# Performance work log

Hardware: AMD Instinct MI355X
Metric: run time of the kernel (lower is better)

## Reference

```python
import jax, jax.numpy as jnp
import numpy as np

ARITY = 4
DEPTH = 8  # leaves live at level DEPTH; levels 0..DEPTH, BFS layout
N_NODES = (ARITY ** (DEPTH + 1) - 1) // (ARITY - 1)  # 87381
V, E, H = 1024, 128, 128


def _offset(level):
    return (ARITY ** level - 1) // (ARITY - 1)


def _lstm_final(seq, w_ih, w_hh, b):
    # seq: [T, B, E_in] -> final hidden state [B, H] (torch LSTM cell, gate order i,f,g,o)
    B = seq.shape[1]
    Hh = w_hh.shape[1]
    xg = jnp.einsum('tbe,ge->tbg', seq, w_ih) + b  # precompute input projections [T,B,4H]

    def step(carry, g_t):
        h, c = carry
        g = g_t + h @ w_hh.T
        i, f, gg, o = jnp.split(g, 4, axis=-1)
        c = jax.nn.sigmoid(f) * c + jax.nn.sigmoid(i) * jnp.tanh(gg)
        h = jax.nn.sigmoid(o) * jnp.tanh(c)
        return (h, c), None

    init = (jnp.zeros((B, Hh), seq.dtype), jnp.zeros((B, Hh), seq.dtype))
    (h, _), _ = jax.lax.scan(step, init, xg)
    return h


def setup_inputs():
    key = jax.random.key(0)
    ks = jax.random.split(key, 12)
    s = 0.1
    labels = jax.random.randint(ks[0], (N_NODES,), 0, V)
    emb = jax.random.normal(ks[1], (V, E), jnp.float32) * s
    emb = emb.at[0].set(0.0)  # padding_idx=0
    mk = lambda k, shp: jax.random.normal(k, shp, jnp.float32) * s
    return {
        'labels': labels, 'emb': emb,
        'w_ih_f': mk(ks[2], (4 * H, E)), 'w_hh_f': mk(ks[3], (4 * H, H)),
        'b_ih_f': mk(ks[4], (4 * H,)), 'b_hh_f': mk(ks[5], (4 * H,)),
        'w_ih_b': mk(ks[6], (4 * H, E)), 'w_hh_b': mk(ks[7], (4 * H, H)),
        'b_ih_b': mk(ks[8], (4 * H,)), 'b_hh_b': mk(ks[9], (4 * H,)),
        'lin_w': mk(ks[10], (E, 2 * H)), 'lin_b': mk(ks[11], (E,)),
    }


def reference(labels, emb, w_ih_f, w_hh_f, b_ih_f, b_hh_f,
              w_ih_b, w_hh_b, b_ih_b, b_hh_b, lin_w, lin_b):
    # padding row is frozen at zero (padding_idx=0 semantics)
    emb = emb.at[0].set(0.0)
    node_emb = emb[labels]  # [N, E]
    bf = b_ih_f + b_hh_f
    bb = b_ih_b + b_hh_b
    enc = jnp.zeros((N_NODES, E), node_emb.dtype)
    # level-by-level dynamic batching: identical math to per-node recursion
    for level in range(DEPTH, -1, -1):
        start = _offset(level)
        count = ARITY ** level
        x = node_emb[start:start + count]  # [C, E]
        if level == DEPTH:
            seq = jnp.stack([x, x])  # leaves: [node, node] -> [2, C, E]
        else:
            cstart = _offset(level + 1)
            ch = enc[cstart:cstart + count * ARITY]
            ch = ch.reshape(count, ARITY, E).transpose(1, 0, 2)  # [K, C, E]
            seq = jnp.concatenate([x[None], ch, x[None]], axis=0)  # [K+2, C, E]
        h_f = _lstm_final(seq, w_ih_f, w_hh_f, bf)          # forward direction
        h_b = _lstm_final(seq[::-1], w_ih_b, w_hh_b, bb)    # reverse direction
        out = jnp.tanh(jnp.concatenate([h_f, h_b], axis=-1) @ lin_w.T + lin_b)
        enc = enc.at[start:start + count].set(out)
    return enc[0]  # root encoding, shape [E]
```

## Files before the change

### kernel.cpp

```cpp
#include <hip/hip_runtime.h>
#include <hip/hip_bf16.h>

typedef __attribute__((ext_vector_type(8))) short bf16x8;
typedef __attribute__((ext_vector_type(4))) float f32x4;

__device__ __forceinline__ ushort f2bf(float f) {
  union { float f; unsigned u; } v; v.f = f;
  unsigned u = v.u;
  return (ushort)((u + 0x7FFFu + ((u >> 16) & 1u)) >> 16);
}
__device__ __forceinline__ float bf2f(ushort u) {
  union { unsigned u; float f; } v; v.u = ((unsigned)u) << 16;
  return v.f;
}
__device__ __forceinline__ float fsig(float x) {
  return __builtin_amdgcn_rcpf(1.0f + __expf(-x));
}
__device__ __forceinline__ float ftnh(float x) {
  float e = __expf(2.0f * x);
  return 1.0f - 2.0f * __builtin_amdgcn_rcpf(e + 1.0f);
}
__device__ __forceinline__ f32x4 MF(bf16x8 a, bf16x8 b, f32x4 c) {
  return __builtin_amdgcn_mfma_f32_16x16x32_bf16(a, b, c, 0, 0, 0);
}

__global__ __launch_bounds__(256) void repack_all2(
    const float* __restrict__ wihf, const float* __restrict__ whhf,
    const float* __restrict__ wihb, const float* __restrict__ whhb,
    const float* __restrict__ emb, const float* __restrict__ linw,
    ushort* __restrict__ wall) {
  int i = blockIdx.x * 256 + threadIdx.x;
  if (i < 131072) {
    int e = i & 7, f = (i >> 3) & 15, lane = (i >> 7) & 63, w = (i >> 13) & 7,
        d = (i >> 16) & 1;
    int nt = f >> 2, kk = f & 3;
    int pcol = w * 64 + nt * 16 + (lane & 15);
    int g = (pcol >> 4) & 3, h = (pcol >> 6) * 16 + (pcol & 15);
    int k = kk * 32 + (lane >> 4) * 8 + e;
    const float* src = d ? whhb : whhf;
    wall[i] = f2bf(src[(g * 128 + h) * 128 + k]);
  } else if (i < 262144) {
    int r = i - 131072;
    int e = r & 7, lane = (r >> 3) & 63, kk = (r >> 9) & 3, j = (r >> 11) & 7,
        wq = (r >> 14) & 3, d = (r >> 16) & 1;
    int pcol = wq * 128 + j * 16 + (lane & 15);
    int g = (pcol >> 4) & 3, h = (pcol >> 6) * 16 + (pcol & 15);
    int k = kk * 32 + (lane >> 4) * 8 + e;
    const float* src = d ? wihb : wihf;
    wall[i] = f2bf(src[(g * 128 + h) * 128 + k]);
  } else if (i < 294912) {
    int r = i - 262144;
    int e = r & 7, lane = (r >> 3) & 63, kk = (r >> 9) & 7, w = (r >> 12) & 7;
    int col = w * 16 + (lane & 15);
    int k = kk * 32 + (lane >> 4) * 8 + e;
    wall[i] = f2bf(linw[col * 256 + k]);
  } else if (i < 425984) {
    int r = i - 294912;
    wall[i] = f2bf(emb[r]);
  }
}

__global__ __launch_bounds__(512) void vocab_all(
    const ushort* __restrict__ emb_bf, const ushort* __restrict__ wihrep,
    const ushort* __restrict__ whhrep, const ushort* __restrict__ linrep,
    const float* __restrict__ linb, const float* __restrict__ bihf,
    const float* __restrict__ bhhf, const float* __restrict__ bihb,
    const float* __restrict__ bhhb, ushort* __restrict__ gxv,
    ushort* __restrict__ gcv) {
  __shared__ __align__(16) ushort sT[2048];
  __shared__ __align__(16) ushort sGx[16384];
  __shared__ __align__(16) ushort sHf[2][2048];
  __shared__ __align__(16) ushort sH[2048];
  const int tid = threadIdx.x;
  const int w = tid >> 6, l = tid & 63, hlo = l & 15, lg = l >> 4;
  const int r0 = lg * 4, k0 = lg * 8;
  const int hcol = w * 16 + hlo;
  const int v0 = blockIdx.x * 16;

  {
    int row = tid >> 5, col0 = (tid & 31) * 4;
    *(ushort4*)(sT + row * 128 + (col0 ^ ((row & 7) << 3))) =
        *(const ushort4*)(emb_bf + (size_t)(v0 + row) * 128 + col0);
  }
  __syncthreads();
  const int dd = w >> 2, wq = w & 3;
  {
    const ushort* wp = wihrep + (size_t)(dd * 4 + wq) * 16384 + l * 8;
    bf16x8 wfv[32];
#pragma unroll
    for (int j = 0; j < 8; ++j)
#pragma unroll
      for (int kk = 0; kk < 4; ++kk)
        wfv[j * 4 + kk] = *(const bf16x8*)(wp + j * 2048 + kk * 512);
    bf16x8 a[4];
#pragma unroll
    for (int kk = 0; kk < 4; ++kk)
      a[kk] = *(const bf16x8*)(sT + hlo * 128 + ((kk * 32 + k0) ^ ((hlo & 7) << 3)));
    f32x4 acc[8];
#pragma unroll
    for (int j = 0; j < 8; ++j) { f32x4 z = {0.f, 0.f, 0.f, 0.f}; acc[j] = z; }
#pragma unroll
    for (int kk = 0; kk < 4; ++kk)
#pragma unroll
      for (int j = 0; j < 8; ++j) acc[j] = MF(a[kk], wfv[j * 4 + kk], acc[j]);
#pragma unroll
    for (int p = 0; p < 2; ++p)
#pragma unroll
      for (int rg = 0; rg < 4; ++rg) {
        int hid = (wq * 2 + p) * 16 + hlo;
        ushort4 q = {f2bf(acc[p * 4 + 0][rg]), f2bf(acc[p * 4 + 1][rg]),
                     f2bf(acc[p * 4 + 2][rg]), f2bf(acc[p * 4 + 3][rg])};
        *(ushort4*)(gxv + (size_t)(v0 + r0 + rg) * 1024 + dd * 512 + hid * 4) = q;
        *(ushort4*)(sGx + (r0 + rg) * 1024 + dd * 512 + hid * 4) = q;
      }
  }
  __syncthreads();

  for (int d = 0; d < 2; ++d) {
    bf16x8 whh[16];
    {
      const ushort* p = whhrep + d * 65536 + w * 8192 + l * 128;
#pragma unroll
      for (int f = 0; f < 16; ++f) whh[f] = *(const bf16x8*)(p + f * 8);
    }
    const float* bih = d ? bihb : bihf;
    const float* bhh = d ? bhhb : bhhf;
    float bs[4];
#pragma unroll
    for (int nt = 0; nt < 4; ++nt)
      bs[nt] = bih[nt * 128 + hcol] + bhh[nt * 128 + hcol];
    ushort4 xg[4];
#pragma unroll
    for (int rg = 0; rg < 4; ++rg)
      xg[rg] = *(const ushort4*)(sGx + (r0 + rg) * 1024 + d * 512 + hcol * 4);
    float c_st[4], hn[4];
#pragma unroll
    for (int rg = 0; rg < 4; ++rg) {
      float g0 = bf2f(xg[rg].x) + bs[0];
      float g2 = bf2f(xg[rg].z) + bs[2];
      float g3 = bf2f(xg[rg].w) + bs[3];
      float c = fsig(g0) * ftnh(g2);
      c_st[rg] = c;
      hn[rg] = fsig(g3) * ftnh(c);
    }
#pragma unroll
    for (int rg = 0; rg < 4; ++rg) {
      int rr = r0 + rg;
      sH[rr * 128 + (hcol ^ ((rr & 7) << 3))] = f2bf(hn[rg]);
    }
    __syncthreads();
    f32x4 a4[4];
#pragma unroll
    for (int rg = 0; rg < 4; ++rg)
#pragma unroll
      for (int nt = 0; nt < 4; ++nt)
        a4[nt][rg] = bf2f(((const ushort*)&xg[rg])[nt]) + bs[nt];
    bf16x8 ah[4];
#pragma unroll
    for (int kk = 0; kk < 4; ++kk)
      ah[kk] = *(const bf16x8*)(sH + hlo * 128 + ((kk * 32 + k0) ^ ((hlo & 7) << 3)));
#pragma unroll
    for (int kk = 0; kk < 4; ++kk)
#pragma unroll
      for (int nt = 0; nt < 4; ++nt) a4[nt] = MF(ah[kk], whh[nt * 4 + kk], a4[nt]);
#pragma unroll
    for (int rg = 0; rg < 4; ++rg) {
      float iv = fsig(a4[0][rg]);
      float fv = fsig(a4[1][rg]);
      float gv = ftnh(a4[2][rg]);
      float ov = fsig(a4[3][rg]);
      float c = fv * c_st[rg] + iv * gv;
      int rr = r0 + rg;
      sHf[d][rr * 128 + (hcol ^ ((rr & 7) << 3))] = f2bf(ov * ftnh(c));
    }
    __syncthreads();
  }

  {
    const float lb = linb[hcol];
    f32x4 hac = {lb, lb, lb, lb};
#pragma unroll
    for (int kk = 0; kk < 8; ++kk) {
      bf16x8 lfr = *(const bf16x8*)(linrep + w * 4096 + kk * 512 + l * 8);
      bf16x8 af = *(const bf16x8*)(&sHf[kk >> 2][0] + hlo * 128 +
                                   (((kk & 3) * 32 + k0) ^ ((hlo & 7) << 3)));
      hac = MF(af, lfr, hac);
    }
#pragma unroll
    for (int rg = 0; rg < 4; ++rg) {
      int rr = r0 + rg;
      sT[rr * 128 + (hcol ^ ((rr & 7) << 3))] = f2bf(ftnh(hac[rg]));
    }
    __syncthreads();
    const ushort* wp = wihrep + (size_t)(dd * 4 + wq) * 16384 + l * 8;
    bf16x8 a[4];
#pragma unroll
    for (int kk = 0; kk < 4; ++kk)
      a[kk] = *(const bf16x8*)(sT + hlo * 128 + ((kk * 32 + k0) ^ ((hlo & 7) << 3)));
    f32x4 acc[8];
#pragma unroll
    for (int j = 0; j < 8; ++j) { f32x4 z = {0.f, 0.f, 0.f, 0.f}; acc[j] = z; }
#pragma unroll
    for (int kk = 0; kk < 4; ++kk)
#pragma unroll
      for (int j = 0; j < 8; ++j) {
        bf16x8 wf = *(const bf16x8*)(wp + j * 2048 + kk * 512);
        acc[j] = MF(a[kk], wf, acc[j]);
      }
#pragma unroll
    for (int p = 0; p < 2; ++p)
#pragma unroll
      for (int rg = 0; rg < 4; ++rg) {
        int hid = (wq * 2 + p) * 16 + hlo;
        ushort4 q = {f2bf(acc[p * 4 + 0][rg]), f2bf(acc[p * 4 + 1][rg]),
                     f2bf(acc[p * 4 + 2][rg]), f2bf(acc[p * 4 + 3][rg])};
        *(ushort4*)(gcv + (size_t)(v0 + r0 + rg) * 1024 + dd * 512 + hid * 4) = q;
      }
  }
}

template <int MT, bool CLAB>
__global__ __launch_bounds__(512, 1) void scan_lvl3(
    const int* __restrict__ xlab, const int* __restrict__ clab,
    const ushort* __restrict__ gxv, const ushort* __restrict__ gsrc,
    const ushort* __restrict__ wihrep, const ushort* __restrict__ whhrep,
    const ushort* __restrict__ linrep, const float* __restrict__ linb,
    const float* __restrict__ bihf, const float* __restrict__ bhhf,
    const float* __restrict__ bihb, const float* __restrict__ bhhb,
    ushort* __restrict__ gdst) {
  __shared__ __align__(16) ushort sH[2][MT * 2048];
  __shared__ __align__(16) ushort sHF[2][MT * 2048];
  __shared__ __align__(16) ushort sT[2048];
  __shared__ int sLabX[MT * 16];
  __shared__ int sLabC[CLAB ? MT * 64 : 1];

  const int tid = threadIdx.x;
  const int w = tid >> 6, l = tid & 63, hlo = l & 15, lg = l >> 4;
  const int r0 = lg * 4, k0 = lg * 8;
  const int hcol = w * 16 + hlo;
  const int axswz = (hlo & 7) << 3;
  const int n0 = blockIdx.x * (MT * 16);

  for (int i = tid; i < MT * 16; i += 512) sLabX[i] = xlab[n0 + i];
  if (CLAB)
    for (int i = tid; i < MT * 64; i += 512) sLabC[i] = clab[4 * n0 + i];
  __syncthreads();

  for (int d = 0; d < 2; ++d) {
    bf16x8 whh[16];
    {
      const ushort* p = whhrep + d * 65536 + w * 8192 + l * 128;
#pragma unroll
      for (int f = 0; f < 16; ++f) whh[f] = *(const bf16x8*)(p + f * 8);
    }
    const float* bih = d ? bihb : bihf;
    const float* bhh = d ? bhhb : bhhf;
    float bs[4];
#pragma unroll
    for (int nt = 0; nt < 4; ++nt)
      bs[nt] = bih[nt * 128 + hcol] + bhh[nt * 128 + hcol];

    float c_st[MT][4];
#pragma unroll
    for (int mt = 0; mt < MT; ++mt) {
      ushort4 xg[4];
#pragma unroll
      for (int rg = 0; rg < 4; ++rg) {
        int ln = mt * 16 + r0 + rg;
        xg[rg] = *(const ushort4*)(gxv + (size_t)sLabX[ln] * 1024 + d * 512 +
                                   hcol * 4);
      }
#pragma unroll
      for (int rg = 0; rg < 4; ++rg) {
        float g0 = bf2f(xg[rg].x) + bs[0];
        float g2 = bf2f(xg[rg].z) + bs[2];
        float g3 = bf2f(xg[rg].w) + bs[3];
        float c = fsig(g0) * ftnh(g2);
        c_st[mt][rg] = c;
        float h = fsig(g3) * ftnh(c);
        int rr = r0 + rg;
        sH[0][mt * 2048 + rr * 128 + (hcol ^ ((rr & 7) << 3))] = f2bf(h);
      }
    }
    __syncthreads();

#pragma unroll
    for (int t = 1; t < 6; ++t) {
      ushort4 gv[MT][4];
      if (t < 5) {
        const int ci = d ? (4 - t) : (t - 1);
#pragma unroll
        for (int mt = 0; mt < MT; ++mt)
#pragma unroll
          for (int rg = 0; rg < 4; ++rg) {
            int ln = mt * 16 + r0 + rg;
            size_t row =
                CLAB ? (size_t)sLabC[ln * 4 + ci] : (size_t)(4 * (n0 + ln) + ci);
            gv[mt][rg] = *(const ushort4*)(gsrc + row * 1024 + d * 512 + hcol * 4);
          }
      } else {
#pragma unroll
        for (int mt = 0; mt < MT; ++mt)
#pragma unroll
          for (int rg = 0; rg < 4; ++rg) {
            int ln = mt * 16 + r0 + rg;
            gv[mt][rg] = *(const ushort4*)(gxv + (size_t)sLabX[ln] * 1024 +
                                           d * 512 + hcol * 4);
          }
      }
#pragma unroll
      for (int mt = 0; mt < MT; ++mt) {
        f32x4 a4[4];
#pragma unroll
        for (int nt = 0; nt < 4; ++nt) {
          f32x4 z = {bs[nt], bs[nt], bs[nt], bs[nt]};
          a4[nt] = z;
        }
        bf16x8 ah[4];
#pragma unroll
        for (int kk = 0; kk < 4; ++kk)
          ah[kk] = *(const bf16x8*)(&sH[(t + 1) & 1][mt * 2048] + hlo * 128 +
                                    ((kk * 32 + k0) ^ axswz));
#pragma unroll
        for (int kk = 0; kk < 4; ++kk)
#pragma unroll
          for (int nt = 0; nt < 4; ++nt)
            a4[nt] = MF(ah[kk], whh[nt * 4 + kk], a4[nt]);
#pragma unroll
        for (int rg = 0; rg < 4; ++rg) {
          a4[0][rg] += bf2f(gv[mt][rg].x);
          a4[1][rg] += bf2f(gv[mt][rg].y);
          a4[2][rg] += bf2f(gv[mt][rg].z);
          a4[3][rg] += bf2f(gv[mt][rg].w);
        }
        float hn[4];
#pragma unroll
        for (int rg = 0; rg < 4; ++rg) {
          float iv = fsig(a4[0][rg]);
          float fv = fsig(a4[1][rg]);
          float gg = ftnh(a4[2][rg]);
          float ov = fsig(a4[3][rg]);
          float c = fv * c_st[mt][rg] + iv * gg;
          c_st[mt][rg] = c;
          hn[rg] = ov * ftnh(c);
        }
        ushort* dstp =
            (t < 5) ? &sH[t & 1][mt * 2048] : &sHF[d][mt * 2048];
#pragma unroll
        for (int rg = 0; rg < 4; ++rg) {
          int rr = r0 + rg;
          dstp[rr * 128 + (hcol ^ ((rr & 7) << 3))] = f2bf(hn[rg]);
        }
      }
      __syncthreads();
    }
  }

  const int dd = w >> 2, wq = w & 3;
  const float lb = linb[hcol];
  bf16x8 lf[8];
#pragma unroll
  for (int kk = 0; kk < 8; ++kk)
    lf[kk] = *(const bf16x8*)(linrep + w * 4096 + kk * 512 + l * 8);
#pragma unroll
  for (int mt = 0; mt < MT; ++mt) {
    f32x4 hac = {lb, lb, lb, lb};
#pragma unroll
    for (int kk = 0; kk < 8; ++kk) {
      bf16x8 af = *(const bf16x8*)(&sHF[kk >> 2][mt * 2048] + hlo * 128 +
                                   (((kk & 3) * 32 + k0) ^ axswz));
      hac = MF(af, lf[kk], hac);
    }
    __syncthreads();
#pragma unroll
    for (int rg = 0; rg < 4; ++rg) {
      int rr = r0 + rg;
      sT[rr * 128 + (hcol ^ ((rr & 7) << 3))] = f2bf(ftnh(hac[rg]));
    }
    __syncthreads();
    bf16x8 a[4];
#pragma unroll
    for (int kk = 0; kk < 4; ++kk)
      a[kk] = *(const bf16x8*)(sT + hlo * 128 + ((kk * 32 + k0) ^ axswz));
#pragma unroll
    for (int half = 0; half < 2; ++half) {
      const ushort* wp = wihrep + (size_t)(dd * 4 + wq) * 16384 +
                         (size_t)(half * 4) * 2048 + l * 8;
      f32x4 acc[4];
#pragma unroll
      for (int j = 0; j < 4; ++j) { f32x4 z = {0.f, 0.f, 0.f, 0.f}; acc[j] = z; }
#pragma unroll
      for (int kk = 0; kk < 4; ++kk)
#pragma unroll
        for (int j = 0; j < 4; ++j) {
          bf16x8 wf = *(const bf16x8*)(wp + j * 2048 + kk * 512);
          acc[j] = MF(a[kk], wf, acc[j]);
        }
      const int hid = (wq * 2 + half) * 16 + hlo;
#pragma unroll
      for (int rg = 0; rg < 4; ++rg) {
        int n = n0 + mt * 16 + r0 + rg;
        ushort4 q = {f2bf(acc[0][rg]), f2bf(acc[1][rg]), f2bf(acc[2][rg]),
                     f2bf(acc[3][rg])};
        *(ushort4*)(gdst + (size_t)n * 1024 + dd * 512 + hid * 4) = q;
      }
    }
  }
}

__global__ __launch_bounds__(512) void tail_lvls(
    const int* __restrict__ labels, const ushort* __restrict__ gxv,
    const ushort* __restrict__ gc3, const ushort* __restrict__ wihrep,
    const ushort* __restrict__ whhrep, const ushort* __restrict__ linrep,
    const float* __restrict__ linb, const float* __restrict__ bihf,
    const float* __restrict__ bhhf, const float* __restrict__ bihb,
    const float* __restrict__ bhhb, float* __restrict__ outp) {
  __shared__ __align__(16) ushort sH[2][2048];
  __shared__ __align__(16) ushort sHF[2][2048];
  __shared__ __align__(16) ushort sT[2048];
  __shared__ __align__(16) ushort sGc[16384];

  const int tid = threadIdx.x;
  const int w = tid >> 6, l = tid & 63, hlo = l & 15, lg = l >> 4;
  const int r0 = lg * 4, k0 = lg * 8;
  const int hcol = w * 16 + hlo;
  const int axswz = (hlo & 7) << 3;
  const int dd = w >> 2, wq = w & 3;

  bf16x8 lf[8];
#pragma unroll
  for (int kk = 0; kk < 8; ++kk)
    lf[kk] = *(const bf16x8*)(linrep + w * 4096 + kk * 512 + l * 8);
  const float lb = linb[hcol];
  const int cnts[3] = {16, 4, 1};
  const int xoffs[3] = {5, 1, 0};

  for (int p = 0; p < 3; ++p) {
    const int cnt = cnts[p];
    const int* xlab = labels + xoffs[p];
    const ushort* gsrc = (p == 0) ? gc3 : (const ushort*)sGc;
    int nnr[4];
#pragma unroll
    for (int rg = 0; rg < 4; ++rg) {
      int n = r0 + rg;
      nnr[rg] = (n < cnt) ? n : (cnt - 1);
    }

    for (int d = 0; d < 2; ++d) {
      bf16x8 whh[16];
      {
        const ushort* pw = whhrep + d * 65536 + w * 8192 + l * 128;
#pragma unroll
        for (int f = 0; f < 16; ++f) whh[f] = *(const bf16x8*)(pw + f * 8);
      }
      const float* bih = d ? bihb : bihf;
      const float* bhh = d ? bhhb : bhhf;
      float bs[4];
#pragma unroll
      for (int nt = 0; nt < 4; ++nt)
        bs[nt] = bih[nt * 128 + hcol] + bhh[nt * 128 + hcol];

      ushort4 xg[4];
#pragma unroll
      for (int rg = 0; rg < 4; ++rg)
        xg[rg] = *(const ushort4*)(gxv + (size_t)xlab[nnr[rg]] * 1024 +
                                   d * 512 + hcol * 4);
      float c_st[4];
#pragma unroll
      for (int t = 0; t < 6; ++t) {
        const bool isx = (t == 0) || (t == 5);
        f32x4 a4[4];
#pragma unroll
        for (int rg = 0; rg < 4; ++rg) {
          ushort4 u;
          if (isx) {
            u = xg[rg];
          } else {
            const int ci = d ? (4 - t) : (t - 1);
            int row = 4 * nnr[rg] + ci;
            u = *(const ushort4*)(gsrc + (size_t)row * 1024 + d * 512 + hcol * 4);
          }
#pragma unroll
          for (int nt = 0; nt < 4; ++nt)
            a4[nt][rg] = bf2f(((const ushort*)&u)[nt]) + bs[nt];
        }
        if (t > 0) {
          bf16x8 ah[4];
#pragma unroll
          for (int kk = 0; kk < 4; ++kk)
            ah[kk] = *(const bf16x8*)(&sH[(t + 1) & 1][0] + hlo * 128 +
                                      ((kk * 32 + k0) ^ axswz));
#pragma unroll
          for (int kk = 0; kk < 4; ++kk)
#pragma unroll
            for (int nt = 0; nt < 4; ++nt)
              a4[nt] = MF(ah[kk], whh[nt * 4 + kk], a4[nt]);
        }
        float hn[4];
#pragma unroll
        for (int rg = 0; rg < 4; ++rg) {
          float iv = fsig(a4[0][rg]);
          float fv = fsig(a4[1][rg]);
          float gv = ftnh(a4[2][rg]);
          float ov = fsig(a4[3][rg]);
          float c = (t == 0) ? (iv * gv) : (fv * c_st[rg] + iv * gv);
          c_st[rg] = c;
          hn[rg] = ov * ftnh(c);
        }
        ushort* dstp = (t < 5) ? &sH[t & 1][0] : &sHF[d][0];
#pragma unroll
        for (int rg = 0; rg < 4; ++rg) {
          int rr = r0 + rg;
          dstp[rr * 128 + (hcol ^ ((rr & 7) << 3))] = f2bf(hn[rg]);
        }
        __syncthreads();
      }
    }

    f32x4 hac = {lb, lb, lb, lb};
#pragma unroll
    for (int kk = 0; kk < 8; ++kk) {
      bf16x8 af = *(const bf16x8*)(&sHF[kk >> 2][0] + hlo * 128 +
                                   (((kk & 3) * 32 + k0) ^ axswz));
      hac = MF(af, lf[kk], hac);
    }
    if (p == 2) {
      if (lg == 0) outp[hcol] = ftnh(hac[0]);
      return;
    }
    __syncthreads();
#pragma unroll
    for (int rg = 0; rg < 4; ++rg) {
      int rr = r0 + rg;
      sT[rr * 128 + (hcol ^ ((rr & 7) << 3))] = f2bf(ftnh(hac[rg]));
    }
    __syncthreads();
    bf16x8 a[4];
#pragma unroll
    for (int kk = 0; kk < 4; ++kk)
      a[kk] = *(const bf16x8*)(sT + hlo * 128 + ((kk * 32 + k0) ^ axswz));
    f32x4 acc[8];
#pragma unroll
    for (int j = 0; j < 8; ++j) { f32x4 z = {0.f, 0.f, 0.f, 0.f}; acc[j] = z; }
    const ushort* wp = wihrep + (size_t)(dd * 4 + wq) * 16384 + l * 8;
#pragma unroll
    for (int kk = 0; kk < 4; ++kk)
#pragma unroll
      for (int j = 0; j < 8; ++j) {
        bf16x8 wf = *(const bf16x8*)(wp + j * 2048 + kk * 512);
        acc[j] = MF(a[kk], wf, acc[j]);
      }
#pragma unroll
    for (int pp = 0; pp < 2; ++pp)
#pragma unroll
      for (int rg = 0; rg < 4; ++rg) {
        int n = r0 + rg;
        if (n < cnt) {
          int hid = (wq * 2 + pp) * 16 + hlo;
          ushort4 q = {f2bf(acc[pp * 4 + 0][rg]), f2bf(acc[pp * 4 + 1][rg]),
                       f2bf(acc[pp * 4 + 2][rg]), f2bf(acc[pp * 4 + 3][rg])};
          *(ushort4*)(sGc + (size_t)n * 1024 + dd * 512 + hid * 4) = q;
        }
      }
    __syncthreads();
  }
}

extern "C" void kernel_launch(void* const* d_in, const int* in_sizes, int n_in,
                              void* d_out, int out_size, void* d_ws, size_t ws_size,
                              hipStream_t stream) {
  const int* labels = (const int*)d_in[0];
  const float* emb = (const float*)d_in[1];
  const float* w_ih_f = (const float*)d_in[2];
  const float* w_hh_f = (const float*)d_in[3];
  const float* b_ih_f = (const float*)d_in[4];
  const float* b_hh_f = (const float*)d_in[5];
  const float* w_ih_b = (const float*)d_in[6];
  const float* w_hh_b = (const float*)d_in[7];
  const float* b_ih_b = (const float*)d_in[8];
  const float* b_hh_b = (const float*)d_in[9];
  const float* lin_w = (const float*)d_in[10];
  const float* lin_b = (const float*)d_in[11];
  float* out = (float*)d_out;

  ushort* gxv = (ushort*)d_ws;
  ushort* gcA = gxv + 1048576;
  ushort* gcB = gcA + 16777216;
  ushort* gcv = gcB;
  ushort* wall = gcB + 4194304;
  ushort* whhrep = wall;
  ushort* wihrep = wall + 131072;
  ushort* linrep = wall + 262144;
  ushort* emb_bf = wall + 294912;

  repack_all2<<<1664, 256, 0, stream>>>(w_ih_f, w_hh_f, w_ih_b, w_hh_b, emb,
                                        lin_w, wall);
  vocab_all<<<64, 512, 0, stream>>>(emb_bf, wihrep, whhrep, linrep, lin_b,
                                    b_ih_f, b_hh_f, b_ih_b, b_hh_b, gxv, gcv);
  scan_lvl3<4, true><<<256, 512, 0, stream>>>(
      labels + 5461, labels + 21845, gxv, gcv, wihrep, whhrep, linrep, lin_b,
      b_ih_f, b_hh_f, b_ih_b, b_hh_b, gcA);
  scan_lvl3<1, false><<<256, 512, 0, stream>>>(
      labels + 1365, nullptr, gxv, gcA, wihrep, whhrep, linrep, lin_b, b_ih_f,
      b_hh_f, b_ih_b, b_hh_b, gcB);
  scan_lvl3<1, false><<<64, 512, 0, stream>>>(
      labels + 341, nullptr, gxv, gcB, wihrep, whhrep, linrep, lin_b, b_ih_f,
      b_hh_f, b_ih_b, b_hh_b, gcA);
  scan_lvl3<1, false><<<16, 512, 0, stream>>>(
      labels + 85, nullptr, gxv, gcA, wihrep, whhrep, linrep, lin_b, b_ih_f,
      b_hh_f, b_ih_b, b_hh_b, gcB);
  scan_lvl3<1, false><<<4, 512, 0, stream>>>(
      labels + 21, nullptr, gxv, gcB, wihrep, whhrep, linrep, lin_b, b_ih_f,
      b_hh_f, b_ih_b, b_hh_b, gcA);
  tail_lvls<<<1, 512, 0, stream>>>(labels, gxv, gcA, wihrep, whhrep, linrep,
                                   lin_b, b_ih_f, b_hh_f, b_ih_b, b_hh_b, out);
}
```

Baseline: 272.5 us.

## Prefetch next step's gate inputs and raise occupancy in level scan kernel

The scan kernel now loads the gathered child/input gate rows for the next timestep while the current step's MFMA and gate math run, instead of loading them at the top of each step. This hides global gather latency behind compute. Launch bounds move to two blocks per CU, and the deepest level uses MT=2 with twice as many blocks. The costs are extra registers for the double-buffered gate values and MT=2, which could cause spills under the tighter register cap, plus smaller per-block work.

```diff
diff --git a/kernel.cpp b/kernel.cpp
--- a/kernel.cpp
+++ b/kernel.cpp
@@ -220,7 +220,7 @@
 }
 
 template <int MT, bool CLAB>
-__global__ __launch_bounds__(512, 1) void scan_lvl3(
+__global__ __launch_bounds__(512, 2) void scan_lvl4(
     const int* __restrict__ xlab, const int* __restrict__ clab,
     const ushort* __restrict__ gxv, const ushort* __restrict__ gsrc,
     const ushort* __restrict__ wihrep, const ushort* __restrict__ whhrep,
@@ -261,6 +261,8 @@
       bs[nt] = bih[nt * 128 + hcol] + bhh[nt * 128 + hcol];
 
     float c_st[MT][4];
+    ushort4 gv[MT][4];
+
 #pragma unroll
     for (int mt = 0; mt < MT; ++mt) {
       ushort4 xg[4];
@@ -282,13 +284,25 @@
         sH[0][mt * 2048 + rr * 128 + (hcol ^ ((rr & 7) << 3))] = f2bf(h);
       }
     }
+    {
+      const int ci = d ? 3 : 0;
+#pragma unroll
+      for (int mt = 0; mt < MT; ++mt)
+#pragma unroll
+        for (int rg = 0; rg < 4; ++rg) {
+          int ln = mt * 16 + r0 + rg;
+          size_t row =
+              CLAB ? (size_t)sLabC[ln * 4 + ci] : (size_t)(4 * (n0 + ln) + ci);
+          gv[mt][rg] = *(const ushort4*)(gsrc + row * 1024 + d * 512 + hcol * 4);
+        }
+    }
     __syncthreads();
 
 #pragma unroll
     for (int t = 1; t < 6; ++t) {
-      ushort4 gv[MT][4];
-      if (t < 5) {
-        const int ci = d ? (4 - t) : (t - 1);
+      ushort4 gvn[MT][4];
+      if (t < 4) {
+        const int ci = d ? (3 - t) : t;
 #pragma unroll
         for (int mt = 0; mt < MT; ++mt)
 #pragma unroll
@@ -296,16 +310,17 @@
             int ln = mt * 16 + r0 + rg;
             size_t row =
                 CLAB ? (size_t)sLabC[ln * 4 + ci] : (size_t)(4 * (n0 + ln) + ci);
-            gv[mt][rg] = *(const ushort4*)(gsrc + row * 1024 + d * 512 + hcol * 4);
+            gvn[mt][rg] =
+                *(const ushort4*)(gsrc + row * 1024 + d * 512 + hcol * 4);
           }
-      } else {
+      } else if (t == 4) {
 #pragma unroll
         for (int mt = 0; mt < MT; ++mt)
 #pragma unroll
           for (int rg = 0; rg < 4; ++rg) {
             int ln = mt * 16 + r0 + rg;
-            gv[mt][rg] = *(const ushort4*)(gxv + (size_t)sLabX[ln] * 1024 +
-                                           d * 512 + hcol * 4);
+            gvn[mt][rg] = *(const ushort4*)(gxv + (size_t)sLabX[ln] * 1024 +
+                                            d * 512 + hcol * 4);
           }
       }
 #pragma unroll
@@ -344,13 +359,18 @@
           c_st[mt][rg] = c;
           hn[rg] = ov * ftnh(c);
         }
-        ushort* dstp =
-            (t < 5) ? &sH[t & 1][mt * 2048] : &sHF[d][mt * 2048];
+        ushort* dstp = (t < 5) ? &sH[t & 1][mt * 2048] : &sHF[d][mt * 2048];
 #pragma unroll
         for (int rg = 0; rg < 4; ++rg) {
           int rr = r0 + rg;
           dstp[rr * 128 + (hcol ^ ((rr & 7) << 3))] = f2bf(hn[rg]);
         }
+      }
+      if (t < 5) {
+#pragma unroll
+        for (int mt = 0; mt < MT; ++mt)
+#pragma unroll
+          for (int rg = 0; rg < 4; ++rg) gv[mt][rg] = gvn[mt][rg];
       }
       __syncthreads();
     }
@@ -597,19 +617,19 @@
                                         lin_w, wall);
   vocab_all<<<64, 512, 0, stream>>>(emb_bf, wihrep, whhrep, linrep, lin_b,
                                     b_ih_f, b_hh_f, b_ih_b, b_hh_b, gxv, gcv);
-  scan_lvl3<4, true><<<256, 512, 0, stream>>>(
+  scan_lvl4<2, true><<<512, 512, 0, stream>>>(
       labels + 5461, labels + 21845, gxv, gcv, wihrep, whhrep, linrep, lin_b,
       b_ih_f, b_hh_f, b_ih_b, b_hh_b, gcA);
-  scan_lvl3<1, false><<<256, 512, 0, stream>>>(
+  scan_lvl4<1, false><<<256, 512, 0, stream>>>(
       labels + 1365, nullptr, gxv, gcA, wihrep, whhrep, linrep, lin_b, b_ih_f,
       b_hh_f, b_ih_b, b_hh_b, gcB);
-  scan_lvl3<1, false><<<64, 512, 0, stream>>>(
+  scan_lvl4<1, false><<<64, 512, 0, stream>>>(
       labels + 341, nullptr, gxv, gcB, wihrep, whhrep, linrep, lin_b, b_ih_f,
       b_hh_f, b_ih_b, b_hh_b, gcA);
-  scan_lvl3<1, false><<<16, 512, 0, stream>>>(
+  scan_lvl4<1, false><<<16, 512, 0, stream>>>(
       labels + 85, nullptr, gxv, gcA, wihrep, whhrep, linrep, lin_b, b_ih_f,
       b_hh_f, b_ih_b, b_hh_b, gcB);
-  scan_lvl3<1, false><<<4, 512, 0, stream>>>(
+  scan_lvl4<1, false><<<4, 512, 0, stream>>>(
       labels + 21, nullptr, gxv, gcB, wihrep, whhrep, linrep, lin_b, b_ih_f,
       b_hh_f, b_ih_b, b_hh_b, gcA);
   tail_lvls<<<1, 512, 0, stream>>>(labels, gxv, gcA, wihrep, whhrep, linrep,
```

New measurement: 268.5 us. About the same (-1.5%).

## Run forward and backward LSTM directions concurrently in 1024-thread blocks

Applied to the files above, without the earlier changes.

Doubles the block size to 1024 threads so that waves 0-7 run the forward LSTM direction and waves 8-15 run the backward one at the same time, instead of one after the other. Each direction gets its own double-buffered hidden-state shared memory. The input-projection epilogue is split across all 16 waves by half, so each wave does half the MFMAs and stores it did before. This halves the serial recurrence chain per level, which matters most for the small tail levels. The cost is higher register pressure per block: launch_bounds changes from (512,1) to (1024), and each wave keeps 16 W_hh fragments plus its state.

```diff
diff --git a/kernel.cpp b/kernel.cpp
--- a/kernel.cpp
+++ b/kernel.cpp
@@ -220,7 +220,7 @@
 }
 
 template <int MT, bool CLAB>
-__global__ __launch_bounds__(512, 1) void scan_lvl3(
+__global__ __launch_bounds__(1024) void scan_lvl5(
     const int* __restrict__ xlab, const int* __restrict__ clab,
     const ushort* __restrict__ gxv, const ushort* __restrict__ gsrc,
     const ushort* __restrict__ wihrep, const ushort* __restrict__ whhrep,
@@ -228,135 +228,137 @@
     const float* __restrict__ bihf, const float* __restrict__ bhhf,
     const float* __restrict__ bihb, const float* __restrict__ bhhb,
     ushort* __restrict__ gdst) {
-  __shared__ __align__(16) ushort sH[2][MT * 2048];
+  __shared__ __align__(16) ushort sH[2][2][MT * 2048];
   __shared__ __align__(16) ushort sHF[2][MT * 2048];
   __shared__ __align__(16) ushort sT[2048];
   __shared__ int sLabX[MT * 16];
   __shared__ int sLabC[CLAB ? MT * 64 : 1];
 
   const int tid = threadIdx.x;
-  const int w = tid >> 6, l = tid & 63, hlo = l & 15, lg = l >> 4;
+  const int w16 = tid >> 6;
+  const int d = w16 >> 3;
+  const int w = w16 & 7;
+  const int l = tid & 63, hlo = l & 15, lg = l >> 4;
   const int r0 = lg * 4, k0 = lg * 8;
   const int hcol = w * 16 + hlo;
   const int axswz = (hlo & 7) << 3;
   const int n0 = blockIdx.x * (MT * 16);
 
-  for (int i = tid; i < MT * 16; i += 512) sLabX[i] = xlab[n0 + i];
+  for (int i = tid; i < MT * 16; i += 1024) sLabX[i] = xlab[n0 + i];
   if (CLAB)
-    for (int i = tid; i < MT * 64; i += 512) sLabC[i] = clab[4 * n0 + i];
+    for (int i = tid; i < MT * 64; i += 1024) sLabC[i] = clab[4 * n0 + i];
   __syncthreads();
 
-  for (int d = 0; d < 2; ++d) {
-    bf16x8 whh[16];
-    {
-      const ushort* p = whhrep + d * 65536 + w * 8192 + l * 128;
-#pragma unroll
-      for (int f = 0; f < 16; ++f) whh[f] = *(const bf16x8*)(p + f * 8);
-    }
-    const float* bih = d ? bihb : bihf;
-    const float* bhh = d ? bhhb : bhhf;
-    float bs[4];
-#pragma unroll
-    for (int nt = 0; nt < 4; ++nt)
-      bs[nt] = bih[nt * 128 + hcol] + bhh[nt * 128 + hcol];
-
-    float c_st[MT][4];
+  bf16x8 whh[16];
+  {
+    const ushort* p = whhrep + d * 65536 + w * 8192 + l * 128;
+#pragma unroll
+    for (int f = 0; f < 16; ++f) whh[f] = *(const bf16x8*)(p + f * 8);
+  }
+  const float* bih = d ? bihb : bihf;
+  const float* bhh = d ? bhhb : bhhf;
+  float bs[4];
+#pragma unroll
+  for (int nt = 0; nt < 4; ++nt)
+    bs[nt] = bih[nt * 128 + hcol] + bhh[nt * 128 + hcol];
+
+  float c_st[MT][4];
+#pragma unroll
+  for (int mt = 0; mt < MT; ++mt) {
+    ushort4 xg[4];
+#pragma unroll
+    for (int rg = 0; rg < 4; ++rg) {
+      int ln = mt * 16 + r0 + rg;
+      xg[rg] = *(const ushort4*)(gxv + (size_t)sLabX[ln] * 1024 + d * 512 +
+                                 hcol * 4);
+    }
+#pragma unroll
+    for (int rg = 0; rg < 4; ++rg) {
+      float g0 = bf2f(xg[rg].x) + bs[0];
+      float g2 = bf2f(xg[rg].z) + bs[2];
+      float g3 = bf2f(xg[rg].w) + bs[3];
+      float c = fsig(g0) * ftnh(g2);
+      c_st[mt][rg] = c;
+      float h = fsig(g3) * ftnh(c);
+      int rr = r0 + rg;
+      sH[d][0][mt * 2048 + rr * 128 + (hcol ^ ((rr & 7) << 3))] = f2bf(h);
+    }
+  }
+  __syncthreads();
+
+#pragma unroll
+  for (int t = 1; t < 6; ++t) {
+    ushort4 gv[MT][4];
+    if (t < 5) {
+      const int ci = d ? (4 - t) : (t - 1);
+#pragma unroll
+      for (int mt = 0; mt < MT; ++mt)
+#pragma unroll
+        for (int rg = 0; rg < 4; ++rg) {
+          int ln = mt * 16 + r0 + rg;
+          size_t row =
+              CLAB ? (size_t)sLabC[ln * 4 + ci] : (size_t)(4 * (n0 + ln) + ci);
+          gv[mt][rg] = *(const ushort4*)(gsrc + row * 1024 + d * 512 + hcol * 4);
+        }
+    } else {
+#pragma unroll
+      for (int mt = 0; mt < MT; ++mt)
+#pragma unroll
+        for (int rg = 0; rg < 4; ++rg) {
+          int ln = mt * 16 + r0 + rg;
+          gv[mt][rg] = *(const ushort4*)(gxv + (size_t)sLabX[ln] * 1024 +
+                                         d * 512 + hcol * 4);
+        }
+    }
 #pragma unroll
     for (int mt = 0; mt < MT; ++mt) {
-      ushort4 xg[4];
-#pragma unroll
-      for (int rg = 0; rg < 4; ++rg) {
-        int ln = mt * 16 + r0 + rg;
-        xg[rg] = *(const ushort4*)(gxv + (size_t)sLabX[ln] * 1024 + d * 512 +
-                                   hcol * 4);
-      }
-#pragma unroll
-      for (int rg = 0; rg < 4; ++rg) {
-        float g0 = bf2f(xg[rg].x) + bs[0];
-        float g2 = bf2f(xg[rg].z) + bs[2];
-        float g3 = bf2f(xg[rg].w) + bs[3];
-        float c = fsig(g0) * ftnh(g2);
+      f32x4 a4[4];
+#pragma unroll
+      for (int nt = 0; nt < 4; ++nt) {
+        f32x4 z = {bs[nt], bs[nt], bs[nt], bs[nt]};
+        a4[nt] = z;
+      }
+      bf16x8 ah[4];
+#pragma unroll
+      for (int kk = 0; kk < 4; ++kk)
+        ah[kk] = *(const bf16x8*)(&sH[d][(t + 1) & 1][mt * 2048] + hlo * 128 +
+                                  ((kk * 32 + k0) ^ axswz));
+#pragma unroll
+      for (int kk = 0; kk < 4; ++kk)
+#pragma unroll
+        for (int nt = 0; nt < 4; ++nt)
+          a4[nt] = MF(ah[kk], whh[nt * 4 + kk], a4[nt]);
+#pragma unroll
+      for (int rg = 0; rg < 4; ++rg) {
+        a4[0][rg] += bf2f(gv[mt][rg].x);
+        a4[1][rg] += bf2f(gv[mt][rg].y);
+        a4[2][rg] += bf2f(gv[mt][rg].z);
+        a4[3][rg] += bf2f(gv[mt][rg].w);
+      }
+      float hn[4];
+#pragma unroll
+      for (int rg = 0; rg < 4; ++rg) {
+        float iv = fsig(a4[0][rg]);
+        float fv = fsig(a4[1][rg]);
+        float gg = ftnh(a4[2][rg]);
+        float ov = fsig(a4[3][rg]);
+        float c = fv * c_st[mt][rg] + iv * gg;
         c_st[mt][rg] = c;
-        float h = fsig(g3) * ftnh(c);
+        hn[rg] = ov * ftnh(c);
+      }
+      ushort* dstp =
+          (t < 5) ? &sH[d][t & 1][mt * 2048] : &sHF[d][mt * 2048];
+#pragma unroll
+      for (int rg = 0; rg < 4; ++rg) {
         int rr = r0 + rg;
-        sH[0][mt * 2048 + rr * 128 + (hcol ^ ((rr & 7) << 3))] = f2bf(h);
-      }
-    }
-    __syncthreads();
-
-#pragma unroll
-    for (int t = 1; t < 6; ++t) {
-      ushort4 gv[MT][4];
-      if (t < 5) {
-        const int ci = d ? (4 - t) : (t - 1);
-#pragma unroll
-        for (int mt = 0; mt < MT; ++mt)
-#pragma unroll
-          for (int rg = 0; rg < 4; ++rg) {
-            int ln = mt * 16 + r0 + rg;
-            size_t row =
-                CLAB ? (size_t)sLabC[ln * 4 + ci] : (size_t)(4 * (n0 + ln) + ci);
-            gv[mt][rg] = *(const ushort4*)(gsrc + row * 1024 + d * 512 + hcol * 4);
-          }
-      } else {
-#pragma unroll
-        for (int mt = 0; mt < MT; ++mt)
-#pragma unroll
-          for (int rg = 0; rg < 4; ++rg) {
-            int ln = mt * 16 + r0 + rg;
-            gv[mt][rg] = *(const ushort4*)(gxv + (size_t)sLabX[ln] * 1024 +
-                                           d * 512 + hcol * 4);
-          }
-      }
-#pragma unroll
-      for (int mt = 0; mt < MT; ++mt) {
-        f32x4 a4[4];
-#pragma unroll
-        for (int nt = 0; nt < 4; ++nt) {
-          f32x4 z = {bs[nt], bs[nt], bs[nt], bs[nt]};
-          a4[nt] = z;
-        }
-        bf16x8 ah[4];
-#pragma unroll
-        for (int kk = 0; kk < 4; ++kk)
-          ah[kk] = *(const bf16x8*)(&sH[(t + 1) & 1][mt * 2048] + hlo * 128 +
-                                    ((kk * 32 + k0) ^ axswz));
-#pragma unroll
-        for (int kk = 0; kk < 4; ++kk)
-#pragma unroll
-          for (int nt = 0; nt < 4; ++nt)
-            a4[nt] = MF(ah[kk], whh[nt * 4 + kk], a4[nt]);
-#pragma unroll
-        for (int rg = 0; rg < 4; ++rg) {
-          a4[0][rg] += bf2f(gv[mt][rg].x);
-          a4[1][rg] += bf2f(gv[mt][rg].y);
-          a4[2][rg] += bf2f(gv[mt][rg].z);
-          a4[3][rg] += bf2f(gv[mt][rg].w);
-        }
-        float hn[4];
-#pragma unroll
-        for (int rg = 0; rg < 4; ++rg) {
-          float iv = fsig(a4[0][rg]);
-          float fv = fsig(a4[1][rg]);
-          float gg = ftnh(a4[2][rg]);
-          float ov = fsig(a4[3][rg]);
-          float c = fv * c_st[mt][rg] + iv * gg;
-          c_st[mt][rg] = c;
-          hn[rg] = ov * ftnh(c);
-        }
-        ushort* dstp =
-            (t < 5) ? &sH[t & 1][mt * 2048] : &sHF[d][mt * 2048];
-#pragma unroll
-        for (int rg = 0; rg < 4; ++rg) {
-          int rr = r0 + rg;
-          dstp[rr * 128 + (hcol ^ ((rr & 7) << 3))] = f2bf(hn[rg]);
-        }
-      }
-      __syncthreads();
-    }
-  }
-
-  const int dd = w >> 2, wq = w & 3;
+        dstp[rr * 128 + (hcol ^ ((rr & 7) << 3))] = f2bf(hn[rg]);
+      }
+    }
+    __syncthreads();
+  }
+
+  const int wq = (w16 >> 1) & 3;
+  const int half = w16 & 1;
   const float lb = linb[hcol];
   bf16x8 lf[8];
 #pragma unroll
@@ -372,60 +374,76 @@
       hac = MF(af, lf[kk], hac);
     }
     __syncthreads();
-#pragma unroll
-    for (int rg = 0; rg < 4; ++rg) {
-      int rr = r0 + rg;
-      sT[rr * 128 + (hcol ^ ((rr & 7) << 3))] = f2bf(ftnh(hac[rg]));
+    if (w16 < 8) {
+#pragma unroll
+      for (int rg = 0; rg < 4; ++rg) {
+        int rr = r0 + rg;
+        sT[rr * 128 + (hcol ^ ((rr & 7) << 3))] = f2bf(ftnh(hac[rg]));
+      }
     }
     __syncthreads();
     bf16x8 a[4];
 #pragma unroll
     for (int kk = 0; kk < 4; ++kk)
       a[kk] = *(const bf16x8*)(sT + hlo * 128 + ((kk * 32 + k0) ^ axswz));
-#pragma unroll
-    for (int half = 0; half < 2; ++half) {
-      const ushort* wp = wihrep + (size_t)(dd * 4 + wq) * 16384 +
-                         (size_t)(half * 4) * 2048 + l * 8;
-      f32x4 acc[4];
-#pragma unroll
-      for (int j = 0; j < 4; ++j) { f32x4 z = {0.f, 0.f, 0.f, 0.f}; acc[j] = z; }
-#pragma unroll
-      for (int kk = 0; kk < 4; ++kk)
-#pragma unroll
-        for (int j = 0; j < 4; ++j) {
-          bf16x8 wf = *(const bf16x8*)(wp + j * 2048 + kk * 512);
-          acc[j] = MF(a[kk], wf, acc[j]);
-        }
-      const int hid = (wq * 2 + half) * 16 + hlo;
-#pragma unroll
-      for (int rg = 0; rg < 4; ++rg) {
-        int n = n0 + mt * 16 + r0 + rg;
-        ushort4 q = {f2bf(acc[0][rg]), f2bf(acc[1][rg]), f2bf(acc[2][rg]),
-                     f2bf(acc[3][rg])};
-        *(ushort4*)(gdst + (size_t)n * 1024 + dd * 512 + hid * 4) = q;
-      }
-    }
-  }
-}
-
-__global__ __launch_bounds__(512) void tail_lvls(
+    const ushort* wp = wihrep + (size_t)(d * 4 + wq) * 16384 +
+                       (size_t)(half * 4) * 2048 + l * 8;
+    f32x4 acc[4];
+#pragma unroll
+    for (int j = 0; j < 4; ++j) { f32x4 z = {0.f, 0.f, 0.f, 0.f}; acc[j] = z; }
+#pragma unroll
+    for (int kk = 0; kk < 4; ++kk)
+#pragma unroll
+      for (int j = 0; j < 4; ++j) {
+        bf16x8 wf = *(const bf16x8*)(wp + j * 2048 + kk * 512);
+        acc[j] = MF(a[kk], wf, acc[j]);
+      }
+    const int hid = (wq * 2 + half) * 16 + hlo;
+#pragma unroll
+    for (int rg = 0; rg < 4; ++rg) {
+      int n = n0 + mt * 16 + r0 + rg;
+      ushort4 q = {f2bf(acc[0][rg]), f2bf(acc[1][rg]), f2bf(acc[2][rg]),
+                   f2bf(acc[3][rg])};
+      *(ushort4*)(gdst + (size_t)n * 1024 + d * 512 + hid * 4) = q;
+    }
+  }
+}
+
+__global__ __launch_bounds__(1024) void tail_lvls5(
     const int* __restrict__ labels, const ushort* __restrict__ gxv,
     const ushort* __restrict__ gc3, const ushort* __restrict__ wihrep,
     const ushort* __restrict__ whhrep, const ushort* __restrict__ linrep,
     const float* __restrict__ linb, const float* __restrict__ bihf,
     const float* __restrict__ bhhf, const float* __restrict__ bihb,
     const float* __restrict__ bhhb, float* __restrict__ outp) {
-  __shared__ __align__(16) ushort sH[2][2048];
+  __shared__ __align__(16) ushort sH[2][2][2048];
   __shared__ __align__(16) ushort sHF[2][2048];
   __shared__ __align__(16) ushort sT[2048];
   __shared__ __align__(16) ushort sGc[16384];
 
   const int tid = threadIdx.x;
-  const int w = tid >> 6, l = tid & 63, hlo = l & 15, lg = l >> 4;
+  const int w16 = tid >> 6;
+  const int d = w16 >> 3;
+  const int w = w16 & 7;
+  const int l = tid & 63, hlo = l & 15, lg = l >> 4;
   const int r0 = lg * 4, k0 = lg * 8;
   const int hcol = w * 16 + hlo;
   const int axswz = (hlo & 7) << 3;
-  const int dd = w >> 2, wq = w & 3;
+  const int wq = (w16 >> 1) & 3;
+  const int half = w16 & 1;
+
+  bf16x8 whh[16];
+  {
+    const ushort* pw = whhrep + d * 65536 + w * 8192 + l * 128;
+#pragma unroll
+    for (int f = 0; f < 16; ++f) whh[f] = *(const bf16x8*)(pw + f * 8);
+  }
+  const float* bih = d ? bihb : bihf;
+  const float* bhh = d ? bhhb : bhhf;
+  float bs[4];
+#pragma unroll
+  for (int nt = 0; nt < 4; ++nt)
+    bs[nt] = bih[nt * 128 + hcol] + bhh[nt * 128 + hcol];
 
   bf16x8 lf[8];
 #pragma unroll
@@ -446,75 +464,60 @@
       nnr[rg] = (n < cnt) ? n : (cnt - 1);
     }
 
-    for (int d = 0; d < 2; ++d) {
-      bf16x8 whh[16];
-      {
-        const ushort* pw = whhrep + d * 65536 + w * 8192 + l * 128;
-#pragma unroll
-        for (int f = 0; f < 16; ++f) whh[f] = *(const bf16x8*)(pw + f * 8);
-      }
-      const float* bih = d ? bihb : bihf;
-      const float* bhh = d ? bhhb : bhhf;
-      float bs[4];
-#pragma unroll
-      for (int nt = 0; nt < 4; ++nt)
-        bs[nt] = bih[nt * 128 + hcol] + bhh[nt * 128 + hcol];
-
-      ushort4 xg[4];
-#pragma unroll
-      for (int rg = 0; rg < 4; ++rg)
-        xg[rg] = *(const ushort4*)(gxv + (size_t)xlab[nnr[rg]] * 1024 +
-                                   d * 512 + hcol * 4);
-      float c_st[4];
-#pragma unroll
-      for (int t = 0; t < 6; ++t) {
-        const bool isx = (t == 0) || (t == 5);
-        f32x4 a4[4];
-#pragma unroll
-        for (int rg = 0; rg < 4; ++rg) {
-          ushort4 u;
-          if (isx) {
-            u = xg[rg];
-          } else {
-            const int ci = d ? (4 - t) : (t - 1);
-            int row = 4 * nnr[rg] + ci;
-            u = *(const ushort4*)(gsrc + (size_t)row * 1024 + d * 512 + hcol * 4);
-          }
+    ushort4 xg[4];
+#pragma unroll
+    for (int rg = 0; rg < 4; ++rg)
+      xg[rg] = *(const ushort4*)(gxv + (size_t)xlab[nnr[rg]] * 1024 + d * 512 +
+                                 hcol * 4);
+    float c_st[4];
+#pragma unroll
+    for (int t = 0; t < 6; ++t) {
+      const bool isx = (t == 0) || (t == 5);
+      f32x4 a4[4];
+#pragma unroll
+      for (int rg = 0; rg < 4; ++rg) {
+        ushort4 u;
+        if (isx) {
+          u = xg[rg];
+        } else {
+          const int ci = d ? (4 - t) : (t - 1);
+          int row = 4 * nnr[rg] + ci;
+          u = *(const ushort4*)(gsrc + (size_t)row * 1024 + d * 512 + hcol * 4);
+        }
+#pragma unroll
+        for (int nt = 0; nt < 4; ++nt)
+          a4[nt][rg] = bf2f(((const ushort*)&u)[nt]) + bs[nt];
+      }
+      if (t > 0) {
+        bf16x8 ah[4];
+#pragma unroll
+        for (int kk = 0; kk < 4; ++kk)
+          ah[kk] = *(const bf16x8*)(&sH[d][(t + 1) & 1][0] + hlo * 128 +
+                                    ((kk * 32 + k0) ^ axswz));
+#pragma unroll
+        for (int kk = 0; kk < 4; ++kk)
 #pragma unroll
           for (int nt = 0; nt < 4; ++nt)
-            a4[nt][rg] = bf2f(((const ushort*)&u)[nt]) + bs[nt];
-        }
-        if (t > 0) {
-          bf16x8 ah[4];
-#pragma unroll
-          for (int kk = 0; kk < 4; ++kk)
-            ah[kk] = *(const bf16x8*)(&sH[(t + 1) & 1][0] + hlo * 128 +
-                                      ((kk * 32 + k0) ^ axswz));
-#pragma unroll
-          for (int kk = 0; kk < 4; ++kk)
-#pragma unroll
-            for (int nt = 0; nt < 4; ++nt)
-              a4[nt] = MF(ah[kk], whh[nt * 4 + kk], a4[nt]);
-        }
-        float hn[4];
-#pragma unroll
-        for (int rg = 0; rg < 4; ++rg) {
-          float iv = fsig(a4[0][rg]);
-          float fv = fsig(a4[1][rg]);
-          float gv = ftnh(a4[2][rg]);
-          float ov = fsig(a4[3][rg]);
-          float c = (t == 0) ? (iv * gv) : (fv * c_st[rg] + iv * gv);
-          c_st[rg] = c;
-          hn[rg] = ov * ftnh(c);
-        }
-        ushort* dstp = (t < 5) ? &sH[t & 1][0] : &sHF[d][0];
-#pragma unroll
-        for (int rg = 0; rg < 4; ++rg) {
-          int rr = r0 + rg;
-          dstp[rr * 128 + (hcol ^ ((rr & 7) << 3))] = f2bf(hn[rg]);
-        }
-        __syncthreads();
-      }
+            a4[nt] = MF(ah[kk], whh[nt * 4 + kk], a4[nt]);
+      }
+      float hn[4];
+#pragma unroll
+      for (int rg = 0; rg < 4; ++rg) {
+        float iv = fsig(a4[0][rg]);
+        float fv = fsig(a4[1][rg]);
+        float gv = ftnh(a4[2][rg]);
+        float ov = fsig(a4[3][rg]);
+        float c = (t == 0) ? (iv * gv) : (fv * c_st[rg] + iv * gv);
+        c_st[rg] = c;
+        hn[rg] = ov * ftnh(c);
+      }
+      ushort* dstp = (t < 5) ? &sH[d][t & 1][0] : &sHF[d][0];
+#pragma unroll
+      for (int rg = 0; rg < 4; ++rg) {
+        int rr = r0 + rg;
+        dstp[rr * 128 + (hcol ^ ((rr & 7) << 3))] = f2bf(hn[rg]);
+      }
+      __syncthreads();
     }
 
     f32x4 hac = {lb, lb, lb, lb};
@@ -525,43 +528,44 @@
       hac = MF(af, lf[kk], hac);
     }
     if (p == 2) {
-      if (lg == 0) outp[hcol] = ftnh(hac[0]);
+      if (w16 < 8 && lg == 0) outp[hcol] = ftnh(hac[0]);
       return;
     }
     __syncthreads();
-#pragma unroll
-    for (int rg = 0; rg < 4; ++rg) {
-      int rr = r0 + rg;
-      sT[rr * 128 + (hcol ^ ((rr & 7) << 3))] = f2bf(ftnh(hac[rg]));
+    if (w16 < 8) {
+#pragma unroll
+      for (int rg = 0; rg < 4; ++rg) {
+        int rr = r0 + rg;
+        sT[rr * 128 + (hcol ^ ((rr & 7) << 3))] = f2bf(ftnh(hac[rg]));
+      }
     }
     __syncthreads();
     bf16x8 a[4];
 #pragma unroll
     for (int kk = 0; kk < 4; ++kk)
       a[kk] = *(const bf16x8*)(sT + hlo * 128 + ((kk * 32 + k0) ^ axswz));
-    f32x4 acc[8];
-#pragma unroll
-    for (int j = 0; j < 8; ++j) { f32x4 z = {0.f, 0.f, 0.f, 0.f}; acc[j] = z; }
-    const ushort* wp = wihrep + (size_t)(dd * 4 + wq) * 16384 + l * 8;
-#pragma unroll
-    for (int kk = 0; kk < 4; ++kk)
-#pragma unroll
-      for (int j = 0; j < 8; ++j) {
+    const ushort* wp = wihrep + (size_t)(d * 4 + wq) * 16384 +
+                       (size_t)(half * 4) * 2048 + l * 8;
+    f32x4 acc[4];
+#pragma unroll
+    for (int j = 0; j < 4; ++j) { f32x4 z = {0.f, 0.f, 0.f, 0.f}; acc[j] = z; }
+#pragma unroll
+    for (int kk = 0; kk < 4; ++kk)
+#pragma unroll
+      for (int j = 0; j < 4; ++j) {
         bf16x8 wf = *(const bf16x8*)(wp + j * 2048 + kk * 512);
         acc[j] = MF(a[kk], wf, acc[j]);
       }
-#pragma unroll
-    for (int pp = 0; pp < 2; ++pp)
-#pragma unroll
-      for (int rg = 0; rg < 4; ++rg) {
-        int n = r0 + rg;
-        if (n < cnt) {
-          int hid = (wq * 2 + pp) * 16 + hlo;
-          ushort4 q = {f2bf(acc[pp * 4 + 0][rg]), f2bf(acc[pp * 4 + 1][rg]),
-                       f2bf(acc[pp * 4 + 2][rg]), f2bf(acc[pp * 4 + 3][rg])};
-          *(ushort4*)(sGc + (size_t)n * 1024 + dd * 512 + hid * 4) = q;
-        }
-      }
+    const int hid = (wq * 2 + half) * 16 + hlo;
+#pragma unroll
+    for (int rg = 0; rg < 4; ++rg) {
+      int n = r0 + rg;
+      if (n < cnt) {
+        ushort4 q = {f2bf(acc[0][rg]), f2bf(acc[1][rg]), f2bf(acc[2][rg]),
+                     f2bf(acc[3][rg])};
+        *(ushort4*)(sGc + (size_t)n * 1024 + d * 512 + hid * 4) = q;
+      }
+    }
     __syncthreads();
   }
 }
@@ -597,21 +601,21 @@
                                         lin_w, wall);
   vocab_all<<<64, 512, 0, stream>>>(emb_bf, wihrep, whhrep, linrep, lin_b,
                                     b_ih_f, b_hh_f, b_ih_b, b_hh_b, gxv, gcv);
-  scan_lvl3<4, true><<<256, 512, 0, stream>>>(
+  scan_lvl5<4, true><<<256, 1024, 0, stream>>>(
       labels + 5461, labels + 21845, gxv, gcv, wihrep, whhrep, linrep, lin_b,
       b_ih_f, b_hh_f, b_ih_b, b_hh_b, gcA);
-  scan_lvl3<1, false><<<256, 512, 0, stream>>>(
+  scan_lvl5<1, false><<<256, 1024, 0, stream>>>(
       labels + 1365, nullptr, gxv, gcA, wihrep, whhrep, linrep, lin_b, b_ih_f,
       b_hh_f, b_ih_b, b_hh_b, gcB);
-  scan_lvl3<1, false><<<64, 512, 0, stream>>>(
+  scan_lvl5<1, false><<<64, 1024, 0, stream>>>(
       labels + 341, nullptr, gxv, gcB, wihrep, whhrep, linrep, lin_b, b_ih_f,
       b_hh_f, b_ih_b, b_hh_b, gcA);
-  scan_lvl3<1, false><<<16, 512, 0, stream>>>(
+  scan_lvl5<1, false><<<16, 1024, 0, stream>>>(
       labels + 85, nullptr, gxv, gcA, wihrep, whhrep, linrep, lin_b, b_ih_f,
       b_hh_f, b_ih_b, b_hh_b, gcB);
-  scan_lvl3<1, false><<<4, 512, 0, stream>>>(
+  scan_lvl5<1, false><<<4, 1024, 0, stream>>>(
       labels + 21, nullptr, gxv, gcB, wihrep, whhrep, linrep, lin_b, b_ih_f,
       b_hh_f, b_ih_b, b_hh_b, gcA);
-  tail_lvls<<<1, 512, 0, stream>>>(labels, gxv, gcA, wihrep, whhrep, linrep,
-                                   lin_b, b_ih_f, b_hh_f, b_ih_b, b_hh_b, out);
-}
+  tail_lvls5<<<1, 1024, 0, stream>>>(labels, gxv, gcA, wihrep, whhrep, linrep,
+                                     lin_b, b_ih_f, b_hh_f, b_ih_b, b_hh_b, out);
+}
```

After: 440.5 us. 1.62x slower.
